# Kernel optimization log

Hardware: AMD Instinct MI355X
Metric: run time of the kernel (lower is better)

Reference implementation:

```python
import jax, jax.numpy as jnp
import numpy as np

B, N, C = 16, 576, 1024
H, HD = 16, 64          # num_heads, head_dim
LMAX = 1024             # KV cache capacity
CUR = 256               # pre-existing cur_kv_len
HID = 4096              # mlp hidden
PREFIX = 64             # fixed prefix length from source
EPS = 1e-5


def _ln(x, w, b):
    m = x.mean(-1, keepdims=True)
    v = ((x - m) ** 2).mean(-1, keepdims=True)
    return (x - m) * jax.lax.rsqrt(v + EPS) * w + b


def setup_inputs() -> dict:
    key = jax.random.key(0)
    ks = jax.random.split(key, 8)
    s = 0.02
    return {
        "x": jax.random.normal(ks[0], (B, N, C), jnp.float32),
        "cache_k": jax.random.normal(ks[1], (B, H, LMAX, HD), jnp.float32),
        "cache_v": jax.random.normal(ks[2], (B, H, LMAX, HD), jnp.float32),
        "qkv_w": jax.random.normal(ks[3], (C, 3 * C), jnp.float32) * s,
        "qkv_b": jnp.zeros((3 * C,), jnp.float32),
        "proj_w": jax.random.normal(ks[4], (C, C), jnp.float32) * s,
        "proj_b": jnp.zeros((C,), jnp.float32),
        "norm1_w": jnp.ones((C,), jnp.float32),
        "norm1_b": jnp.zeros((C,), jnp.float32),
        "norm2_w": jnp.ones((C,), jnp.float32),
        "norm2_b": jnp.zeros((C,), jnp.float32),
        "fc1_w": jax.random.normal(ks[5], (C, HID), jnp.float32) * s,
        "fc1_b": jnp.zeros((HID,), jnp.float32),
        "fc2_w": jax.random.normal(ks[6], (HID, C), jnp.float32) * s,
        "fc2_b": jnp.zeros((C,), jnp.float32),
        "cur_kv_len": CUR,
    }


def reference(x, cache_k, cache_v, qkv_w, qkv_b, proj_w, proj_b,
              norm1_w, norm1_b, norm2_w, norm2_b,
              fc1_w, fc1_b, fc2_w, fc2_b, cur_kv_len):
    b, n, c = x.shape
    hd = c // H
    scale = hd ** -0.5

    # ---- attention branch (lazy_mar, not force-fresh) ----
    h = _ln(x, norm1_w, norm1_b)
    qkv = (h @ qkv_w + qkv_b).reshape(b, n, 3, H, hd).transpose(2, 0, 3, 1, 4)
    q, k, v = qkv[0], qkv[1], qkv[2]          # [B,H,N,hd]

    L = cur_kv_len                            # python int -> static slices
    app = n - PREFIX
    # scatter new keys/values into the cache: prefix at [0:64], lazy region appended
    ck = cache_k.at[:, :, PREFIX + L:PREFIX + L + app, :].set(k[:, :, PREFIX:, :])
    ck = ck.at[:, :, :PREFIX, :].set(k[:, :, :PREFIX, :])
    cv = cache_v.at[:, :, PREFIX + L:PREFIX + L + app, :].set(v[:, :, PREFIX:, :])
    cv = cv.at[:, :, :PREFIX, :].set(v[:, :, :PREFIX, :])

    avail = L + n                             # (L + app) + 64
    attn = jax.nn.softmax(
        jnp.einsum('bhqd,bhkd->bhqk', q * scale, ck[:, :, :avail, :]), axis=-1)
    o = jnp.einsum('bhqk,bhkd->bhqd', attn, cv[:, :, :avail, :])
    o = o.transpose(0, 2, 1, 3).reshape(b, n, c)
    x = x + (o @ proj_w + proj_b)

    # ---- MLP branch ----
    h2 = _ln(x, norm2_w, norm2_b)
    mlp = jax.nn.gelu(h2 @ fc1_w + fc1_b, approximate=False) @ fc2_w + fc2_b
    return x + mlp
```

## Files before the change

### kernel.cpp

```cpp
#include <hip/hip_runtime.h>

#define Bb 16
#define Nn_ 576
#define Cc 1024
#define Hh 16
#define HD 64
#define HID 4096
#define AVAIL 832
#define ROWS (Bb*Nn_)

typedef __bf16 bf16x8 __attribute__((ext_vector_type(8)));
typedef float f32x4 __attribute__((ext_vector_type(4)));

__device__ __forceinline__ unsigned short f2bf(float f) {
  unsigned u = __float_as_uint(f);
  u += 0x7FFF + ((u >> 16) & 1);
  return (unsigned short)(u >> 16);
}

__device__ __forceinline__ void glds16(const void* g, void* l) {
  __builtin_amdgcn_global_load_lds(
      (const __attribute__((address_space(1))) void*)g,
      (__attribute__((address_space(3))) void*)l, 16, 0, 0);
}

#define BARR() asm volatile("s_barrier" ::: "memory")
#define VMCNT8() asm volatile("s_waitcnt vmcnt(8)" ::: "memory")
#define VMCNT0() asm volatile("s_waitcnt vmcnt(0)" ::: "memory")
#define LGKM0() asm volatile("s_waitcnt lgkmcnt(0)" ::: "memory")

__global__ void wtrans_k(const float* __restrict__ in, unsigned short* __restrict__ out,
                         int K, int N) {
  __shared__ float tile[32][33];
  int k0 = blockIdx.x * 32, n0 = blockIdx.y * 32;
  int tx = threadIdx.x, ty = threadIdx.y;
#pragma unroll
  for (int i = 0; i < 4; i++)
    tile[ty + i * 8][tx] = in[(size_t)(k0 + ty + i * 8) * N + n0 + tx];
  __syncthreads();
#pragma unroll
  for (int i = 0; i < 4; i++)
    out[(size_t)(n0 + ty + i * 8) * K + k0 + tx] = f2bf(tile[tx][ty + i * 8]);
}

__global__ void ln_k(const float* __restrict__ x, const float* __restrict__ w,
                     const float* __restrict__ bi, unsigned short* __restrict__ out) {
  int row = blockIdx.x;
  int t = threadIdx.x;
  float4 v = ((const float4*)(x + (size_t)row * Cc))[t];
  float s = v.x + v.y + v.z + v.w;
  float s2 = v.x * v.x + v.y * v.y + v.z * v.z + v.w * v.w;
#pragma unroll
  for (int off = 1; off < 64; off <<= 1) { s += __shfl_xor(s, off); s2 += __shfl_xor(s2, off); }
  __shared__ float red[8];
  int wid = t >> 6, lane = t & 63;
  if (lane == 0) { red[wid] = s; red[4 + wid] = s2; }
  __syncthreads();
  s = red[0] + red[1] + red[2] + red[3];
  s2 = red[4] + red[5] + red[6] + red[7];
  float mean = s * (1.0f / Cc);
  float var = s2 * (1.0f / Cc) - mean * mean;
  float rstd = rsqrtf(var + 1e-5f);
  float4 wv = ((const float4*)w)[t];
  float4 bv = ((const float4*)bi)[t];
  ushort4 ov;
  ov.x = f2bf((v.x - mean) * rstd * wv.x + bv.x);
  ov.y = f2bf((v.y - mean) * rstd * wv.y + bv.y);
  ov.z = f2bf((v.z - mean) * rstd * wv.z + bv.z);
  ov.w = f2bf((v.w - mean) * rstd * wv.w + bv.w);
  *(ushort4*)(out + (size_t)row * Cc + t * 4) = ov;
}

template <int EPI>
__global__ __launch_bounds__(512, 2) void gemm8_k(
    const unsigned short* __restrict__ A, const unsigned short* __restrict__ Bt,
    const float* __restrict__ bias, const float* __restrict__ resid,
    void* __restrict__ outv, int N, int K) {
  extern __shared__ __align__(16) char smem[];
  char* A0buf = smem;
  char* B0buf = smem + 32768;
  char* A1buf = smem + 65536;
  char* B1buf = smem + 98304;

  const int tid = threadIdx.x, lane = tid & 63, wid = tid >> 6;
  const int wr = wid >> 2, wc = wid & 3;
  const int l15 = lane & 15, l4 = lane >> 4;
  const int m0 = blockIdx.x * 256, n0 = blockIdx.y * 256;
  const int KT = K >> 6;
  const size_t K2 = (size_t)K * 2;

  const int toff = (tid >> 3) * (int)K2 + ((((tid & 7) ^ ((tid >> 3) & 7)) << 4));
  const char* As0 = (const char*)A + (size_t)m0 * K2 + toff;
  const char* As1 = As0 + 128 * K2;
  const char* Bs0 = (const char*)Bt + (size_t)n0 * K2 + toff;
  const char* Bs1 = Bs0 + 128 * K2;
  const size_t l64 = 64 * K2;
  const int dst = tid * 16;

  const int s0 = ((l4 ^ (l15 & 7)) << 4);
  const int rbA = (wr * 128 + l15) * 128;
  const int rbB = (wc * 64 + l15) * 128;

  f32x4 acc[2][2][4][2] = {};
  bf16x8 a0[4][2], a1[4][2], bb0[2][2], bb1[2][2];

#define STAGE(srcH, ktb, ldsT, half)                        \
  do {                                                      \
    const char* _g = (srcH) + (size_t)(ktb);                \
    glds16(_g, (ldsT) + (half) * 16384 + dst);              \
    glds16(_g + l64, (ldsT) + (half) * 16384 + 8192 + dst); \
  } while (0)

#define RD_A(dA, CA, mh)                                                           \
  _Pragma("unroll") for (int mi = 0; mi < 4; ++mi)                                 \
  _Pragma("unroll") for (int ks = 0; ks < 2; ++ks)                                 \
    dA[mi][ks] = *(const bf16x8*)((CA) + rbA + (mh) * 8192 + mi * 2048 + (s0 ^ (ks << 6)));

#define RD_B(dB, CB, nh)                                                           \
  _Pragma("unroll") for (int ni = 0; ni < 2; ++ni)                                 \
  _Pragma("unroll") for (int ks = 0; ks < 2; ++ks)                                 \
    dB[ni][ks] = *(const bf16x8*)((CB) + rbB + (nh) * 4096 + ni * 2048 + (s0 ^ (ks << 6)));

#define MF(mh, nh, av, bv)                                                         \
  _Pragma("unroll") for (int mi = 0; mi < 4; ++mi)                                 \
  _Pragma("unroll") for (int ni = 0; ni < 2; ++ni)                                 \
  _Pragma("unroll") for (int ks = 0; ks < 2; ++ks)                                 \
    acc[mh][nh][mi][ni] = __builtin_amdgcn_mfma_f32_16x16x32_bf16(                 \
        av[mi][ks], bv[ni][ks], acc[mh][nh][mi][ni], 0, 0, 0);

#define TILE(CA, CB, t)                                             \
  do {                                                              \
    const size_t kt2 = (size_t)((t) + 2) * 128;                     \
                                                            \
    RD_A(a0, CA, 0); RD_B(bb0, CB, 0);                              \
    BARR();                                                         \
    __builtin_amdgcn_s_setprio(1); MF(0, 0, a0, bb0);               \
    __builtin_amdgcn_s_setprio(0); BARR();                          \
                                                            \
    RD_B(bb1, CB, 1);                                               \
    BARR();                                                         \
    __builtin_amdgcn_s_setprio(1); MF(0, 1, a0, bb1);               \
    __builtin_amdgcn_s_setprio(0); BARR();                          \
      \
    RD_A(a1, CA, 1);                                                \
    LGKM0(); BARR();                                                \
    STAGE(As0, kt2, CA, 0);                                         \
    STAGE(As1, kt2, CA, 1);                                         \
    __builtin_amdgcn_s_setprio(1); MF(1, 0, a1, bb0);               \
    __builtin_amdgcn_s_setprio(0); BARR();                          \
                                  \
    STAGE(Bs0, kt2, CB, 0);                                         \
    STAGE(Bs1, kt2, CB, 1);                                         \
    VMCNT8(); BARR();                                               \
    __builtin_amdgcn_s_setprio(1); MF(1, 1, a1, bb1);               \
    __builtin_amdgcn_s_setprio(0); BARR();                          \
  } while (0)

#define TILE_T1(CA, CB)                                             \
  do {                                                              \
    RD_A(a0, CA, 0); RD_B(bb0, CB, 0);                              \
    BARR();                                                         \
    __builtin_amdgcn_s_setprio(1); MF(0, 0, a0, bb0);               \
    __builtin_amdgcn_s_setprio(0); BARR();                          \
    RD_B(bb1, CB, 1);                                               \
    BARR();                                                         \
    __builtin_amdgcn_s_setprio(1); MF(0, 1, a0, bb1);               \
    __builtin_amdgcn_s_setprio(0); BARR();                          \
    RD_A(a1, CA, 1);                                                \
    LGKM0(); BARR();                                                \
    __builtin_amdgcn_s_setprio(1); MF(1, 0, a1, bb0);               \
    __builtin_amdgcn_s_setprio(0); BARR();                          \
    VMCNT0(); BARR();                                               \
    __builtin_amdgcn_s_setprio(1); MF(1, 1, a1, bb1);               \
    __builtin_amdgcn_s_setprio(0); BARR();                          \
  } while (0)

#define TILE_T2(CA, CB)                                             \
  do {                                                              \
    RD_A(a0, CA, 0); RD_A(a1, CA, 1); RD_B(bb0, CB, 0); RD_B(bb1, CB, 1); \
    MF(0, 0, a0, bb0); MF(0, 1, a0, bb1);                           \
    MF(1, 0, a1, bb0); MF(1, 1, a1, bb1);                           \
  } while (0)

  STAGE(As0, 0, A0buf, 0);
  STAGE(As1, 0, A0buf, 1);
  STAGE(Bs0, 0, B0buf, 0);
  STAGE(Bs1, 0, B0buf, 1);
  STAGE(As0, 128, A1buf, 0);
  STAGE(As1, 128, A1buf, 1);
  STAGE(Bs0, 128, B1buf, 0);
  STAGE(Bs1, 128, B1buf, 1);
  VMCNT8();
  BARR();

#pragma unroll 1
  for (int t = 0; t + 3 < KT; t += 2) {
    TILE(A0buf, B0buf, t);
    TILE(A1buf, B1buf, t + 1);
  }
  TILE_T1(A0buf, B0buf);
  TILE_T2(A1buf, B1buf);

  BARR();
  {
    float* eb = (float*)(smem + wid * 16384);
    const int gc0 = n0 + wc * 64;
    const f32x4 bv4 = *(const f32x4*)&bias[gc0 + l15 * 4];
#pragma unroll
    for (int mh = 0; mh < 2; mh++) {
#pragma unroll
      for (int mi = 0; mi < 4; mi++) {
#pragma unroll
        for (int nh = 0; nh < 2; nh++)
#pragma unroll
          for (int ni = 0; ni < 2; ni++)
#pragma unroll
            for (int j = 0; j < 4; j++)
              eb[(l4 * 4 + j) * 68 + nh * 32 + ni * 16 + l15] = acc[mh][nh][mi][ni][j];
        int gr0 = m0 + wr * 128 + mh * 64 + mi * 16;
#pragma unroll
        for (int k = 0; k < 4; k++) {
          int r = k * 4 + l4;
          f32x4 v = *(const f32x4*)&eb[r * 68 + l15 * 4];
          v += bv4;
          size_t base = (size_t)(gr0 + r) * N + gc0 + l15 * 4;
          if (EPI == 1) {
#pragma unroll
            for (int q = 0; q < 4; q++)
              v[q] = 0.5f * v[q] * (1.0f + erff(v[q] * 0.70710678118f));
          }
          if (EPI == 2) {
            f32x4 rv = *(const f32x4*)&resid[base];
            *(f32x4*)((float*)outv + base) = v + rv;
          } else {
            ushort4 o4;
            o4.x = f2bf(v[0]); o4.y = f2bf(v[1]); o4.z = f2bf(v[2]); o4.w = f2bf(v[3]);
            *(ushort4*)((unsigned short*)outv + base) = o4;
          }
        }
      }
    }
  }
#undef TILE_T2
#undef TILE_T1
#undef TILE
#undef MF
#undef RD_B
#undef RD_A
#undef STAGE
}

__global__ void gatherk_k(const unsigned short* __restrict__ qkv,
                          const float* __restrict__ cache_k,
                          unsigned short* __restrict__ Kg) {
  int bh = blockIdx.y, b = bh >> 4, h = bh & 15;
  int p = blockIdx.x * 4 + (threadIdx.x >> 6);
  int d = threadIdx.x & 63;
  unsigned short val;
  if (p < 64)
    val = qkv[((size_t)(b * Nn_ + p)) * 3072 + 1024 + h * 64 + d];
  else if (p < 320)
    val = f2bf(cache_k[(((size_t)b * Hh + h) * 1024 + p) * 64 + d]);
  else
    val = qkv[((size_t)(b * Nn_ + p - 256)) * 3072 + 1024 + h * 64 + d];
  Kg[(((size_t)bh) * AVAIL + p) * 64 + d] = val;
}

__global__ void gathervt_k(const unsigned short* __restrict__ qkv,
                           const float* __restrict__ cache_v,
                           unsigned short* __restrict__ Vt) {
  __shared__ float tile[32][33];
  int bh = blockIdx.z, b = bh >> 4, h = bh & 15;
  int p0 = blockIdx.x * 32, d0 = blockIdx.y * 32;
  int tx = threadIdx.x, ty = threadIdx.y;
#pragma unroll
  for (int i = 0; i < 4; i++) {
    int p = p0 + ty + i * 8, d = d0 + tx;
    float v;
    if (p < 64)
      v = __uint_as_float((unsigned)qkv[((size_t)(b * Nn_ + p)) * 3072 + 2048 + h * 64 + d] << 16);
    else if (p < 320)
      v = cache_v[(((size_t)b * Hh + h) * 1024 + p) * 64 + d];
    else
      v = __uint_as_float((unsigned)qkv[((size_t)(b * Nn_ + p - 256)) * 3072 + 2048 + h * 64 + d] << 16);
    tile[ty + i * 8][tx] = v;
  }
  __syncthreads();
#pragma unroll
  for (int i = 0; i < 4; i++)
    Vt[(((size_t)bh) * 64 + d0 + ty + i * 8) * AVAIL + p0 + tx] = f2bf(tile[tx][ty + i * 8]);
}

__global__ __launch_bounds__(256) void attn_k(
    const unsigned short* __restrict__ qkv, const unsigned short* __restrict__ Kg,
    const unsigned short* __restrict__ Vt, unsigned short* __restrict__ o) {
  __shared__ __attribute__((aligned(16))) unsigned short Qs[64 * 64];
  __shared__ __attribute__((aligned(16))) unsigned short Ks[64 * 64];
  __shared__ __attribute__((aligned(16))) unsigned short Vs[64 * 64];
  __shared__ __attribute__((aligned(16))) unsigned short Ps[4][16 * 64];

  const int tid = threadIdx.x;
  const int lane = tid & 63;
  const int w = tid >> 6;
  const int qt = blockIdx.x;
  const int bh = blockIdx.y, b = bh >> 4, h = bh & 15;
  const float scale = 0.125f;

  {
    int r = tid >> 3;
    int cb = (tid & 7) << 4;
    const char* qb = (const char*)qkv;
    glds16(qb + ((size_t)(b * Nn_ + qt * 64 + r) * 3072 + h * 64) * 2 + cb, (char*)Qs + tid * 16);
    glds16(qb + ((size_t)(b * Nn_ + qt * 64 + 32 + r) * 3072 + h * 64) * 2 + cb,
           (char*)Qs + 4096 + tid * 16);
  }

  float m_run[4], l_run[4];
  f32x4 oacc[4] = {};
#pragma unroll
  for (int j = 0; j < 4; j++) { m_run[j] = -1e30f; l_run[j] = 0.f; }

  const char* kbase = (const char*)(Kg + (size_t)bh * AVAIL * 64);
  const char* vbase = (const char*)(Vt + (size_t)bh * 64 * AVAIL);

  for (int c = 0; c < 13; c++) {
    __syncthreads();
    glds16(kbase + (size_t)c * 8192 + tid * 16, (char*)Ks + tid * 16);
    glds16(kbase + (size_t)c * 8192 + 4096 + tid * 16, (char*)Ks + 4096 + tid * 16);
    {
      int r = tid >> 3;
      int cb = (tid & 7) << 4;
      glds16(vbase + (size_t)r * (AVAIL * 2) + c * 128 + cb, (char*)Vs + tid * 16);
      glds16(vbase + (size_t)(r + 32) * (AVAIL * 2) + c * 128 + cb, (char*)Vs + 4096 + tid * 16);
    }
    asm volatile("s_waitcnt vmcnt(0)" ::: "memory");
    __syncthreads();

    bf16x8 qf[2];
#pragma unroll
    for (int t = 0; t < 2; t++)
      qf[t] = *(const bf16x8*)&Qs[(w * 16 + (lane & 15)) * 64 + t * 32 + (lane >> 4) * 8];
    f32x4 s[4] = {};
#pragma unroll
    for (int nt = 0; nt < 4; nt++) {
#pragma unroll
      for (int t = 0; t < 2; t++) {
        bf16x8 kf = *(const bf16x8*)&Ks[(nt * 16 + (lane & 15)) * 64 + t * 32 + (lane >> 4) * 8];
        s[nt] = __builtin_amdgcn_mfma_f32_16x16x32_bf16(qf[t], kf, s[nt], 0, 0, 0);
      }
    }

    float p[4][4];
#pragma unroll
    for (int j = 0; j < 4; j++) {
      float mx = fmaxf(fmaxf(s[0][j], s[1][j]), fmaxf(s[2][j], s[3][j])) * scale;
#pragma unroll
      for (int off = 1; off < 16; off <<= 1) mx = fmaxf(mx, __shfl_xor(mx, off));
      float m_new = fmaxf(m_run[j], mx);
      float alpha = __expf(m_run[j] - m_new);
      float sum = 0.f;
#pragma unroll
      for (int nt = 0; nt < 4; nt++) {
        p[nt][j] = __expf(s[nt][j] * scale - m_new);
        sum += p[nt][j];
      }
#pragma unroll
      for (int off = 1; off < 16; off <<= 1) sum += __shfl_xor(sum, off);
      l_run[j] = l_run[j] * alpha + sum;
      m_run[j] = m_new;
#pragma unroll
      for (int nt2 = 0; nt2 < 4; nt2++) oacc[nt2][j] *= alpha;
    }

#pragma unroll
    for (int nt = 0; nt < 4; nt++)
#pragma unroll
      for (int j = 0; j < 4; j++)
        Ps[w][((lane >> 4) * 4 + j) * 64 + nt * 16 + (lane & 15)] = f2bf(p[nt][j]);

    bf16x8 pa[2];
#pragma unroll
    for (int t = 0; t < 2; t++)
      pa[t] = *(const bf16x8*)&Ps[w][(lane & 15) * 64 + t * 32 + (lane >> 4) * 8];
#pragma unroll
    for (int nt2 = 0; nt2 < 4; nt2++) {
#pragma unroll
      for (int t = 0; t < 2; t++) {
        bf16x8 vf = *(const bf16x8*)&Vs[(nt2 * 16 + (lane & 15)) * 64 + t * 32 + (lane >> 4) * 8];
        oacc[nt2] = __builtin_amdgcn_mfma_f32_16x16x32_bf16(pa[t], vf, oacc[nt2], 0, 0, 0);
      }
    }
  }

#pragma unroll
  for (int nt2 = 0; nt2 < 4; nt2++) {
#pragma unroll
    for (int j = 0; j < 4; j++) {
      int q = qt * 64 + w * 16 + (lane >> 4) * 4 + j;
      float v = oacc[nt2][j] / l_run[j];
      o[((size_t)(b * Nn_ + q)) * Cc + h * 64 + nt2 * 16 + (lane & 15)] = f2bf(v);
    }
  }
}

extern "C" void kernel_launch(void* const* d_in, const int* in_sizes, int n_in,
                              void* d_out, int out_size, void* d_ws, size_t ws_size,
                              hipStream_t stream) {
  const float* x = (const float*)d_in[0];
  const float* cache_k = (const float*)d_in[1];
  const float* cache_v = (const float*)d_in[2];
  const float* qkv_w = (const float*)d_in[3];
  const float* qkv_b = (const float*)d_in[4];
  const float* proj_w = (const float*)d_in[5];
  const float* proj_b = (const float*)d_in[6];
  const float* n1w = (const float*)d_in[7];
  const float* n1b = (const float*)d_in[8];
  const float* n2w = (const float*)d_in[9];
  const float* n2b = (const float*)d_in[10];
  const float* fc1w = (const float*)d_in[11];
  const float* fc1b = (const float*)d_in[12];
  const float* fc2w = (const float*)d_in[13];
  const float* fc2b = (const float*)d_in[14];

  char* ws = (char*)d_ws;
  unsigned short* wq_t = (unsigned short*)(ws + 0);
  unsigned short* wp_t = (unsigned short*)(ws + 6291456);
  unsigned short* w1_t = (unsigned short*)(ws + 8388608);
  unsigned short* w2_t = (unsigned short*)(ws + 16777216);
  float* x2           = (float*)(ws + 25165824);
  unsigned short* obuf = (unsigned short*)(ws + 62914560);
  unsigned short* hbuf = (unsigned short*)(ws + 81788928);
  unsigned short* vt   = (unsigned short*)(ws + 100663296);
  unsigned short* qkvb = (unsigned short*)(ws + 127926272);
  unsigned short* kg   = (unsigned short*)(ws + 184549376);
  unsigned short* midb = qkvb;

  hipFuncSetAttribute((const void*)&gemm8_k<0>, hipFuncAttributeMaxDynamicSharedMemorySize, 131072);
  hipFuncSetAttribute((const void*)&gemm8_k<1>, hipFuncAttributeMaxDynamicSharedMemorySize, 131072);
  hipFuncSetAttribute((const void*)&gemm8_k<2>, hipFuncAttributeMaxDynamicSharedMemorySize, 131072);

  dim3 b328(32, 8);
  wtrans_k<<<dim3(32, 96), b328, 0, stream>>>(qkv_w, wq_t, 1024, 3072);
  wtrans_k<<<dim3(32, 32), b328, 0, stream>>>(proj_w, wp_t, 1024, 1024);
  wtrans_k<<<dim3(32, 128), b328, 0, stream>>>(fc1w, w1_t, 1024, 4096);
  wtrans_k<<<dim3(128, 32), b328, 0, stream>>>(fc2w, w2_t, 4096, 1024);

  ln_k<<<ROWS, 256, 0, stream>>>(x, n1w, n1b, hbuf);
  gemm8_k<0><<<dim3(36, 12), 512, 131072, stream>>>(hbuf, wq_t, qkv_b, nullptr, qkvb, 3072, 1024);

  gatherk_k<<<dim3(208, 256), 256, 0, stream>>>(qkvb, cache_k, kg);
  gathervt_k<<<dim3(26, 2, 256), b328, 0, stream>>>(qkvb, cache_v, vt);
  attn_k<<<dim3(9, 256), 256, 0, stream>>>(qkvb, kg, vt, obuf);

  gemm8_k<2><<<dim3(36, 4), 512, 131072, stream>>>(obuf, wp_t, proj_b, x, x2, 1024, 1024);
  ln_k<<<ROWS, 256, 0, stream>>>(x2, n2w, n2b, hbuf);
  gemm8_k<1><<<dim3(36, 16), 512, 131072, stream>>>(hbuf, w1_t, fc1b, nullptr, midb, 4096, 1024);
  gemm8_k<2><<<dim3(36, 4), 512, 131072, stream>>>(midb, w2_t, fc2b, x2, (float*)d_out, 1024, 4096);
}
```

Measured before the change: 659.2 us.

## Collapse GEMM tile into one LDS-read phase followed by a single MFMA burst

Replaces the four-phase ping-pong schedule of the GEMM inner tile with a single phase. All A/B fragments are read from LDS up front using explicit ds_read_b128 asm. After a single lgkm wait, barrier and sched_barrier, the next tile's global-to-LDS stages are issued, followed by all 64 MFMAs back to back. This removes most per-tile barriers and priority toggles but raises register pressure (all fragments live at once) and loses the interleaving of LDS reads with MFMA execution.

```diff
diff --git a/kernel.cpp b/kernel.cpp
--- a/kernel.cpp
+++ b/kernel.cpp
@@ -22,6 +22,14 @@
   __builtin_amdgcn_global_load_lds(
       (const __attribute__((address_space(1))) void*)g,
       (__attribute__((address_space(3))) void*)l, 16, 0, 0);
+}
+
+__device__ __forceinline__ bf16x8 ds_read128(const void* p) {
+  bf16x8 r;
+  asm volatile("ds_read_b128 %0, %1"
+               : "=v"(r)
+               : "v"((const __attribute__((address_space(3))) char*)p));
+  return r;
 }
 
 #define BARR() asm volatile("s_barrier" ::: "memory")
@@ -114,12 +122,12 @@
 #define RD_A(dA, CA, mh)                                                           \
   _Pragma("unroll") for (int mi = 0; mi < 4; ++mi)                                 \
   _Pragma("unroll") for (int ks = 0; ks < 2; ++ks)                                 \
-    dA[mi][ks] = *(const bf16x8*)((CA) + rbA + (mh) * 8192 + mi * 2048 + (s0 ^ (ks << 6)));
+    dA[mi][ks] = ds_read128((CA) + rbA + (mh) * 8192 + mi * 2048 + (s0 ^ (ks << 6)));
 
 #define RD_B(dB, CB, nh)                                                           \
   _Pragma("unroll") for (int ni = 0; ni < 2; ++ni)                                 \
   _Pragma("unroll") for (int ks = 0; ks < 2; ++ks)                                 \
-    dB[ni][ks] = *(const bf16x8*)((CB) + rbB + (nh) * 4096 + ni * 2048 + (s0 ^ (ks << 6)));
+    dB[ni][ks] = ds_read128((CB) + rbB + (nh) * 4096 + ni * 2048 + (s0 ^ (ks << 6)));
 
 #define MF(mh, nh, av, bv)                                                         \
   _Pragma("unroll") for (int mi = 0; mi < 4; ++mi)                                 \
@@ -131,53 +139,41 @@
 #define TILE(CA, CB, t)                                             \
   do {                                                              \
     const size_t kt2 = (size_t)((t) + 2) * 128;                     \
-                                                            \
     RD_A(a0, CA, 0); RD_B(bb0, CB, 0);                              \
+    RD_B(bb1, CB, 1); RD_A(a1, CA, 1);                              \
+    LGKM0(); __builtin_amdgcn_sched_barrier(0);                     \
     BARR();                                                         \
-    __builtin_amdgcn_s_setprio(1); MF(0, 0, a0, bb0);               \
-    __builtin_amdgcn_s_setprio(0); BARR();                          \
-                                                            \
-    RD_B(bb1, CB, 1);                                               \
-    BARR();                                                         \
-    __builtin_amdgcn_s_setprio(1); MF(0, 1, a0, bb1);               \
-    __builtin_amdgcn_s_setprio(0); BARR();                          \
-      \
-    RD_A(a1, CA, 1);                                                \
-    LGKM0(); BARR();                                                \
     STAGE(As0, kt2, CA, 0);                                         \
     STAGE(As1, kt2, CA, 1);                                         \
-    __builtin_amdgcn_s_setprio(1); MF(1, 0, a1, bb0);               \
-    __builtin_amdgcn_s_setprio(0); BARR();                          \
-                                  \
     STAGE(Bs0, kt2, CB, 0);                                         \
     STAGE(Bs1, kt2, CB, 1);                                         \
-    VMCNT8(); BARR();                                               \
-    __builtin_amdgcn_s_setprio(1); MF(1, 1, a1, bb1);               \
-    __builtin_amdgcn_s_setprio(0); BARR();                          \
+    __builtin_amdgcn_s_setprio(1);                                  \
+    MF(0, 0, a0, bb0); MF(0, 1, a0, bb1);                           \
+    MF(1, 0, a1, bb0); MF(1, 1, a1, bb1);                           \
+    __builtin_amdgcn_s_setprio(0);                                  \
+    VMCNT8();                                                       \
+    BARR();                                                         \
   } while (0)
 
 #define TILE_T1(CA, CB)                                             \
   do {                                                              \
     RD_A(a0, CA, 0); RD_B(bb0, CB, 0);                              \
+    RD_B(bb1, CB, 1); RD_A(a1, CA, 1);                              \
+    LGKM0(); __builtin_amdgcn_sched_barrier(0);                     \
     BARR();                                                         \
-    __builtin_amdgcn_s_setprio(1); MF(0, 0, a0, bb0);               \
-    __builtin_amdgcn_s_setprio(0); BARR();                          \
-    RD_B(bb1, CB, 1);                                               \
+    __builtin_amdgcn_s_setprio(1);                                  \
+    MF(0, 0, a0, bb0); MF(0, 1, a0, bb1);                           \
+    MF(1, 0, a1, bb0); MF(1, 1, a1, bb1);                           \
+    __builtin_amdgcn_s_setprio(0);                                  \
+    VMCNT0();                                                       \
     BARR();                                                         \
-    __builtin_amdgcn_s_setprio(1); MF(0, 1, a0, bb1);               \
-    __builtin_amdgcn_s_setprio(0); BARR();                          \
-    RD_A(a1, CA, 1);                                                \
-    LGKM0(); BARR();                                                \
-    __builtin_amdgcn_s_setprio(1); MF(1, 0, a1, bb0);               \
-    __builtin_amdgcn_s_setprio(0); BARR();                          \
-    VMCNT0(); BARR();                                               \
-    __builtin_amdgcn_s_setprio(1); MF(1, 1, a1, bb1);               \
-    __builtin_amdgcn_s_setprio(0); BARR();                          \
   } while (0)
 
 #define TILE_T2(CA, CB)                                             \
   do {                                                              \
-    RD_A(a0, CA, 0); RD_A(a1, CA, 1); RD_B(bb0, CB, 0); RD_B(bb1, CB, 1); \
+    RD_A(a0, CA, 0); RD_B(bb0, CB, 0);                              \
+    RD_B(bb1, CB, 1); RD_A(a1, CA, 1);                              \
+    LGKM0(); __builtin_amdgcn_sched_barrier(0);                     \
     MF(0, 0, a0, bb0); MF(0, 1, a0, bb1);                           \
     MF(1, 0, a1, bb0); MF(1, 1, a1, bb1);                           \
   } while (0)
```

New measurement: 763.2 us. 15.8% more time.
